# Kernel tuning notes

Measured on AMD Instinct MI355X. Metric: run time of the kernel, lower is better.

Reference implementation:

```python
import jax, jax.numpy as jnp
import numpy as np

N, E, D_IN, D_OUT = 100000, 1250000, 64, 100


def setup_inputs() -> dict:
    key = jax.random.key(0)
    ks = jax.random.split(key, 12)
    inp = {
        "x": jax.random.normal(ks[0], (N, D_IN), dtype=jnp.float32),
        "edge_index": jax.random.randint(ks[1], (2, E), 0, N, dtype=jnp.int64),
        "edge_weight": jax.random.uniform(ks[2], (E,), dtype=jnp.float32),
        # ChebConv(64,100,K=1): one weight + bias
        "W10": jax.random.normal(ks[3], (D_IN, D_OUT), dtype=jnp.float32) * 0.1,
        "b1": jnp.zeros((D_OUT,), dtype=jnp.float32),
        # ChebConv(64,100,K=2)
        "W20": jax.random.normal(ks[4], (D_IN, D_OUT), dtype=jnp.float32) * 0.1,
        "W21": jax.random.normal(ks[5], (D_IN, D_OUT), dtype=jnp.float32) * 0.1,
        "b2": jnp.zeros((D_OUT,), dtype=jnp.float32),
        # ChebConv(64,100,K=3)
        "W30": jax.random.normal(ks[6], (D_IN, D_OUT), dtype=jnp.float32) * 0.1,
        "W31": jax.random.normal(ks[7], (D_IN, D_OUT), dtype=jnp.float32) * 0.1,
        "W32": jax.random.normal(ks[8], (D_IN, D_OUT), dtype=jnp.float32) * 0.1,
        "b3": jnp.zeros((D_OUT,), dtype=jnp.float32),
    }
    return inp


def _cheb_norm(edge_index, edge_weight, n):
    # PyG ChebConv.__norm__ with normalization='sym', lambda_max=2.0:
    # L_hat = (2/lambda_max) * (I - D^-1/2 A D^-1/2) - I = -D^-1/2 A D^-1/2
    # (the +1 diagonal of L and the -1 self-loop cancel), diag entries are 0.
    row, col = edge_index[0], edge_index[1]
    deg = jax.ops.segment_sum(edge_weight, row, num_segments=n)
    dis = jnp.where(deg > 0, jax.lax.rsqrt(jnp.where(deg > 0, deg, 1.0)), 0.0)
    return -dis[row] * edge_weight * dis[col]


def _cheb_conv(x, edge_index, w_hat, weights, bias):
    # out = sum_k T_k(L_hat) x @ W_k + b, with T0=x, T1=Lx, T_k=2L T_{k-1}-T_{k-2}
    n = x.shape[0]
    row, col = edge_index[0], edge_index[1]

    def prop(t):  # L_hat @ t via edge gather/scatter
        return jax.ops.segment_sum(t[row] * w_hat[:, None], col, num_segments=n)

    tx0 = x
    out = tx0 @ weights[0]
    if len(weights) > 1:
        tx1 = prop(tx0)
        out = out + tx1 @ weights[1]
        for k in range(2, len(weights)):
            tx2 = 2.0 * prop(tx1) - tx0
            out = out + tx2 @ weights[k]
            tx0, tx1 = tx1, tx2
    return out + bias


def reference(x, edge_index, edge_weight, W10, b1, W20, W21, b2, W30, W31, W32, b3):
    w_hat = _cheb_norm(edge_index, edge_weight, x.shape[0])
    s1 = _cheb_conv(x, edge_index, w_hat, [W10], b1)
    s2 = _cheb_conv(x, edge_index, w_hat, [W20, W21], b2)
    s3 = _cheb_conv(x, edge_index, w_hat, [W30, W31, W32], b3)
    return jnp.concatenate([s1, s2, s3], axis=1)  # [N, 300]
```

## Files before the change

kernel.cpp:

```cpp
#include <hip/hip_runtime.h>


typedef __attribute__((ext_vector_type(8))) short short8;
typedef __attribute__((ext_vector_type(8))) unsigned short ushort8;
typedef __attribute__((ext_vector_type(4))) float f32x4;

#define NSBMAX 64
#define NSPLIT 16
#define NSPLIT_ROW 8

__device__ inline float bf2f(unsigned short u) {
    return __uint_as_float(((unsigned int)u) << 16);
}
__device__ inline unsigned short f2bf(float f) {
    unsigned int u = __float_as_uint(f);
    u = (u + 0x7FFF + ((u >> 16) & 1)) >> 16;
    return (unsigned short)u;
}

__global__ __launch_bounds__(512) void partA_kernel(
        const int* __restrict__ row, const int* __restrict__ col,
        const float* __restrict__ ew, int* __restrict__ colAcur,
        int* __restrict__ rowAcur, uint2* __restrict__ colA,
        uint2* __restrict__ rowA, int E, int nsb, int chunk, int capA) {
    __shared__ int hc[NSBMAX];
    __shared__ int hr[NSBMAX];
    const int t = threadIdx.x;
    const int s = blockIdx.x * chunk;
    const int e = min(E, s + chunk);
    if (s >= E) return;
    if (t < NSBMAX) { hc[t] = 0; hr[t] = 0; }
    __syncthreads();
    for (int i = s + t; i < e; i += 512) {
        atomicAdd(&hc[col[i] >> 11], 1);
        atomicAdd(&hr[row[i] >> 11], 1);
    }
    __syncthreads();
    if (t < nsb) {
        int n = hc[t];
        hc[t] = n ? atomicAdd(&colAcur[t], n) : 0;
        n = hr[t];
        hr[t] = n ? atomicAdd(&rowAcur[t], n) : 0;
    }
    __syncthreads();
    for (int i = s + t; i < e; i += 512) {
        int r = row[i], c = col[i];
        float w = ew[i];
        int pc = atomicAdd(&hc[c >> 11], 1);
        if (pc < capA)
            colA[(size_t)(c >> 11) * capA + pc] =
                make_uint2(((unsigned)(c & 2047) << 17) | (unsigned)r, __float_as_uint(w));
        int pr = atomicAdd(&hr[r >> 11], 1);
        if (pr < capA)
            rowA[(size_t)(r >> 11) * capA + pr] = make_uint2((unsigned)r, __float_as_uint(w));
    }
}

__global__ __launch_bounds__(512) void partB_kernel(
        const int* __restrict__ colAcur, const uint2* __restrict__ colA,
        int* __restrict__ colBcur, uint2* __restrict__ colB,
        int capA, int capB) {
    __shared__ int h[8];
    const int sb = blockIdx.x / NSPLIT;
    const int j = blockIdx.x % NSPLIT;
    const int t = threadIdx.x;
    const int cnt = min(colAcur[sb], capA);
    const int chunk = (cnt + NSPLIT - 1) / NSPLIT;
    const int s = j * chunk;
    const int e = min(cnt, s + chunk);
    if (t < 8) h[t] = 0;
    __syncthreads();
    const uint2* part = colA + (size_t)sb * capA;
    for (int i = s + t; i < e; i += 512) atomicAdd(&h[part[i].x >> 25], 1);
    __syncthreads();
    if (t < 8) {
        int n = h[t];
        h[t] = n ? atomicAdd(&colBcur[sb * 8 + t], n) : 0;
    }
    __syncthreads();
    for (int i = s + t; i < e; i += 512) {
        uint2 rec = part[i];
        int f = rec.x >> 25;
        int p = atomicAdd(&h[f], 1);
        if (p < capB) {
            unsigned coff = (rec.x >> 17) & 255u;
            unsigned r = rec.x & 0x1FFFFu;
            colB[(size_t)(sb * 8 + f) * capB + p] = make_uint2((coff << 24) | r, rec.y);
        }
    }
}

__global__ __launch_bounds__(512) void fine_rowp_kernel(
        const int* __restrict__ rowAcur, const uint2* __restrict__ rowA,
        float* __restrict__ partial, int capA) {
    __shared__ float sdeg[2048];
    const int sb = blockIdx.x / NSPLIT_ROW;
    const int j = blockIdx.x % NSPLIT_ROW;
    const int t = threadIdx.x;
    const int cnt = min(rowAcur[sb], capA);
    const int chunk = (cnt + NSPLIT_ROW - 1) / NSPLIT_ROW;
    const int s = j * chunk;
    const int e = min(cnt, s + chunk);
    for (int k = t; k < 2048; k += 512) sdeg[k] = 0.f;
    __syncthreads();
    const uint2* part = rowA + (size_t)sb * capA;
    for (int i = s + t; i < e; i += 512) {
        uint2 rec = part[i];
        atomicAdd(&sdeg[rec.x & 2047u], __uint_as_float(rec.y));
    }
    __syncthreads();
    float* dstp = partial + (size_t)blockIdx.x * 2048;
    for (int k = t; k < 2048; k += 512) dstp[k] = sdeg[k];
}

__global__ void colbase_scan_kernel(const int* __restrict__ colBcur,
                                    int* __restrict__ colbase,
                                    int* __restrict__ rowptr, int N, int nfb, int capB) {
    __shared__ int s[512];
    int t = threadIdx.x;
    int v = (t < nfb) ? min(colBcur[t], capB) : 0;
    s[t] = v;
    __syncthreads();
    for (int o = 1; o < 512; o <<= 1) {
        int u = (t >= o) ? s[t - o] : 0;
        __syncthreads();
        s[t] += u;
        __syncthreads();
    }
    if (t < nfb) colbase[t] = s[t] - v;
    if (t == 511) rowptr[N] = s[511];
}

__global__ __launch_bounds__(256) void fine_col_kernel(
        const int* __restrict__ colBcur, const int* __restrict__ colbase,
        const uint2* __restrict__ colB, const float* __restrict__ dis,
        uint2* __restrict__ erec, int* __restrict__ rowptr, int N, int capB) {
    __shared__ int h[256];
    __shared__ int sc[256];
    __shared__ int cur[256];
    const int b = blockIdx.x, t = threadIdx.x;
    const int sz = min(colBcur[b], capB);
    const uint2* part = colB + (size_t)b * capB;
    h[t] = 0;
    __syncthreads();
    for (int i = t; i < sz; i += 256) atomicAdd(&h[part[i].x >> 24], 1);
    __syncthreads();
    int v = h[t];
    sc[t] = v;
    __syncthreads();
    for (int o = 1; o < 256; o <<= 1) {
        int u = (t >= o) ? sc[t - o] : 0;
        __syncthreads();
        sc[t] += u;
        __syncthreads();
    }
    int excl = sc[t] - v;
    const int base = colbase[b];
    int c = (b << 8) + t;
    if (c < N) rowptr[c] = base + excl;
    cur[t] = excl;
    __syncthreads();
    for (int i = t; i < sz; i += 256) {
        uint2 rec = part[i];
        int coff = rec.x >> 24;
        int r = rec.x & 0xFFFFFFu;
        int pos = atomicAdd(&cur[coff], 1);
        float wd = __uint_as_float(rec.y) * dis[r];
        erec[(size_t)base + pos] = make_uint2((unsigned)r, __float_as_uint(wd));
    }
}

__global__ void deg_count_kernel(const int* __restrict__ row, const int* __restrict__ col,
                                 const float* __restrict__ ew,
                                 float* __restrict__ deg, int* __restrict__ cnt, int E) {
    int e = blockIdx.x * 256 + threadIdx.x;
    if (e < E) {
        atomicAdd(&deg[row[e]], ew[e]);
        atomicAdd(&cnt[col[e]], 1);
    }
}

__global__ void scan1_kernel(const int* __restrict__ cnt, int* __restrict__ pre,
                             int* __restrict__ bsum, int N) {
    __shared__ int s[256];
    int t = threadIdx.x;
    int i = blockIdx.x * 256 + t;
    int v = (i < N) ? cnt[i] : 0;
    s[t] = v;
    __syncthreads();
    for (int o = 1; o < 256; o <<= 1) {
        int u = (t >= o) ? s[t - o] : 0;
        __syncthreads();
        s[t] += u;
        __syncthreads();
    }
    if (i < N) pre[i] = s[t] - v;
    if (t == 255) bsum[blockIdx.x] = s[255];
}

__global__ void scan2_kernel(const int* __restrict__ bsum, int* __restrict__ bpre, int nb) {
    __shared__ int s[512];
    int t = threadIdx.x;
    int v = (t < nb) ? bsum[t] : 0;
    s[t] = v;
    __syncthreads();
    for (int o = 1; o < 512; o <<= 1) {
        int u = (t >= o) ? s[t - o] : 0;
        __syncthreads();
        s[t] += u;
        __syncthreads();
    }
    if (t < nb) bpre[t] = s[t] - v;
}

__global__ void scan3_kernel(int* __restrict__ rowptr, int* __restrict__ cursor,
                             const int* __restrict__ bpre, int N, int E) {
    int i = blockIdx.x * 256 + threadIdx.x;
    if (i < N) {
        int v = rowptr[i] + bpre[i >> 8];
        rowptr[i] = v;
        cursor[i] = v;
    }
    if (i == 0) rowptr[N] = E;
}

__global__ void scatter_compact_kernel(const int* __restrict__ row, const int* __restrict__ col,
                                       const float* __restrict__ ew, int* __restrict__ cursor,
                                       uint2* __restrict__ erec, int E) {
    int e = blockIdx.x * 256 + threadIdx.x;
    if (e < E) {
        int p = atomicAdd(&cursor[col[e]], 1);
        erec[p] = make_uint2((unsigned)row[e], __float_as_uint(ew[e]));
    }
}

__global__ void cvt_dis_kernel(const float* __restrict__ x, unsigned short* __restrict__ xb,
                               const float* __restrict__ degp, float* __restrict__ dis,
                               int N, int total4, int mode) {
    int i = blockIdx.x * 256 + threadIdx.x;
    if (i < total4) {
        float4 v = reinterpret_cast<const float4*>(x)[i];
        ushort4 o;
        o.x = f2bf(v.x); o.y = f2bf(v.y); o.z = f2bf(v.z); o.w = f2bf(v.w);
        reinterpret_cast<ushort4*>(xb)[i] = o;
    }
    if (mode && i < N) {
        float d;
        if (mode == 2) {
            const float* p = degp + ((size_t)(i >> 11) * NSPLIT_ROW) * 2048 + (i & 2047);
            d = 0.f;
#pragma unroll
            for (int j = 0; j < NSPLIT_ROW; ++j) d += p[(size_t)j * 2048];
        } else {
            d = degp[i];
        }
        dis[i] = (d > 0.f) ? rsqrtf(d) : 0.f;
    }
}

__global__ void gather_kernel(const int* __restrict__ ptr, const uint2* __restrict__ erec,
                              const float* __restrict__ dis,
                              const unsigned short* __restrict__ src,
                              unsigned short* __restrict__ dst, int N, int premul) {
    int node = blockIdx.x * 4 + (threadIdx.x >> 6);
    int lane = threadIdx.x & 63;
    if (node >= N) return;
    int s = ptr[node];
    int d = ptr[node + 1] - s;
    const int h = lane >> 5;
    const int c2 = (lane & 31) * 2;
    float acc0 = 0.f, acc1 = 0.f;
    for (int base = 0; base < d; base += 64) {
        int n = min(64, d - base);
        int ex = 0;
        float w = 0.f;
        if (lane < n) {
            uint2 e = erec[s + base + lane];
            ex = (int)e.x;
            w = __uint_as_float(e.y);
            if (!premul) w *= dis[ex];
        }
        int n8 = (n + 7) & ~7;
        for (int j = 0; j < n8; j += 8) {
            int r0 = __shfl(ex, j + 0, 64), r1 = __shfl(ex, j + 1, 64);
            int r2 = __shfl(ex, j + 2, 64), r3 = __shfl(ex, j + 3, 64);
            int r4 = __shfl(ex, j + 4, 64), r5 = __shfl(ex, j + 5, 64);
            int r6 = __shfl(ex, j + 6, 64), r7 = __shfl(ex, j + 7, 64);
            float w0 = __shfl(w, j + 0, 64), w1 = __shfl(w, j + 1, 64);
            float w2 = __shfl(w, j + 2, 64), w3 = __shfl(w, j + 3, 64);
            float w4 = __shfl(w, j + 4, 64), w5 = __shfl(w, j + 5, 64);
            float w6 = __shfl(w, j + 6, 64), w7 = __shfl(w, j + 7, 64);
            int ra = h ? r1 : r0;  float wa = h ? w1 : w0;
            int rb = h ? r3 : r2;  float wb = h ? w3 : w2;
            int rc = h ? r5 : r4;  float wc = h ? w5 : w4;
            int rd = h ? r7 : r6;  float wd = h ? w7 : w6;
            unsigned va = *reinterpret_cast<const unsigned*>(src + (size_t)ra * 64 + c2);
            unsigned vb = *reinterpret_cast<const unsigned*>(src + (size_t)rb * 64 + c2);
            unsigned vc = *reinterpret_cast<const unsigned*>(src + (size_t)rc * 64 + c2);
            unsigned vd = *reinterpret_cast<const unsigned*>(src + (size_t)rd * 64 + c2);
            acc0 = fmaf(wa, bf2f((unsigned short)(va & 0xFFFFu)), acc0);
            acc1 = fmaf(wa, bf2f((unsigned short)(va >> 16)), acc1);
            acc0 = fmaf(wb, bf2f((unsigned short)(vb & 0xFFFFu)), acc0);
            acc1 = fmaf(wb, bf2f((unsigned short)(vb >> 16)), acc1);
            acc0 = fmaf(wc, bf2f((unsigned short)(vc & 0xFFFFu)), acc0);
            acc1 = fmaf(wc, bf2f((unsigned short)(vc >> 16)), acc1);
            acc0 = fmaf(wd, bf2f((unsigned short)(vd & 0xFFFFu)), acc0);
            acc1 = fmaf(wd, bf2f((unsigned short)(vd >> 16)), acc1);
        }
    }
    acc0 += __shfl_xor(acc0, 32, 64);
    acc1 += __shfl_xor(acc1, 32, 64);
    if (lane < 32) {
        float sc = -dis[node];
        unsigned o = (unsigned)f2bf(sc * acc0) | ((unsigned)f2bf(sc * acc1) << 16);
        *reinterpret_cast<unsigned*>(dst + (size_t)node * 64 + c2) = o;
    }
}

__global__ void prep_w_kernel(const float* __restrict__ W10, const float* __restrict__ W20,
                              const float* __restrict__ W21, const float* __restrict__ W30,
                              const float* __restrict__ W31, const float* __restrict__ W32,
                              unsigned short* __restrict__ imgW) {
    int i = blockIdx.x * 256 + threadIdx.x;
    if (i >= 6 * 7168) return;
    int img = i / 7168;
    int rem = i - img * 7168;
    int j = rem & 7;
    int l = (rem >> 3) & 63;
    int ks = (rem >> 9) & 1;
    int t = rem >> 10;
    const float* W;
    switch (img) {
        case 0: W = W10; break;
        case 1: W = W20; break;
        case 2: W = W21; break;
        case 3: W = W30; break;
        case 4: W = W31; break;
        default: W = W32; break;
    }
    int n = t * 16 + (l & 15);
    int k = ks * 32 + (l >> 4) * 8 + j;
    float v = (n < 100) ? W[k * 100 + n] : 0.f;
    imgW[i] = f2bf(v);
}

#define PRODUCT(AF, IMGOFF, SEGBASE)                                                   \
    do {                                                                               \
        _Pragma("unroll") for (int ks = 0; ks < 2; ++ks) {                             \
            _Pragma("unroll") for (int t = 0; t < 7; ++t) {                            \
                short8 bfr = *reinterpret_cast<const short8*>(                         \
                    imgW + (IMGOFF) + ((t * 2 + ks) << 9) + (l << 3));                 \
                acc[(SEGBASE) + t] = __builtin_amdgcn_mfma_f32_16x16x32_bf16(          \
                    bfr, AF[ks], acc[(SEGBASE) + t], 0, 0, 0);                         \
            }                                                                          \
        }                                                                              \
    } while (0)

__global__ __launch_bounds__(256) void gemm_fused_kernel(
        const unsigned short* __restrict__ xb, const unsigned short* __restrict__ tx1b,
        const unsigned short* __restrict__ p2b, const unsigned short* __restrict__ imgW,
        const float* __restrict__ b1, const float* __restrict__ b2,
        const float* __restrict__ b3, float* __restrict__ out, int N) {
    __shared__ unsigned short Ftx[64 * 64];
    __shared__ unsigned short Ft1[64 * 64];
    __shared__ unsigned short Ft2[64 * 64];
    const int row0 = blockIdx.x * 64;
    const int tid = threadIdx.x;
    const int wv = tid >> 6;
    const int l = tid & 63;
    const int m = l & 15;
    const int q = l >> 4;

    f32x4 acc[21];
#pragma unroll
    for (int t = 0; t < 21; ++t) acc[t] = (f32x4){0.f, 0.f, 0.f, 0.f};

#pragma unroll
    for (int it = 0; it < 2; ++it) {
        int i = tid + it * 256;
        int r = i >> 3, g = i & 7;
        int grow = row0 + r;
        ushort8 vx = {0, 0, 0, 0, 0, 0, 0, 0};
        ushort8 v1 = vx, v2 = vx;
        if (grow < N) {
            vx = *reinterpret_cast<const ushort8*>(xb + (size_t)grow * 64 + g * 8);
            v1 = *reinterpret_cast<const ushort8*>(tx1b + (size_t)grow * 64 + g * 8);
            ushort8 vp = *reinterpret_cast<const ushort8*>(p2b + (size_t)grow * 64 + g * 8);
#pragma unroll
            for (int jj = 0; jj < 8; ++jj)
                v2[jj] = f2bf(2.f * bf2f(vp[jj]) - bf2f(vx[jj]));
        }
        int off = r * 64 + ((g ^ (r & 7)) << 3);
        *reinterpret_cast<ushort8*>(&Ftx[off]) = vx;
        *reinterpret_cast<ushort8*>(&Ft1[off]) = v1;
        *reinterpret_cast<ushort8*>(&Ft2[off]) = v2;
    }
    __syncthreads();

    const int arow = wv * 16 + m;
    short8 ax[2], a1[2], a2[2];
#pragma unroll
    for (int ks = 0; ks < 2; ++ks) {
        int o = arow * 64 + (((ks * 4 + q) ^ (arow & 7)) << 3);
        ax[ks] = *reinterpret_cast<const short8*>(&Ftx[o]);
        a1[ks] = *reinterpret_cast<const short8*>(&Ft1[o]);
        a2[ks] = *reinterpret_cast<const short8*>(&Ft2[o]);
    }

    PRODUCT(ax, 0, 0);
    PRODUCT(ax, 7168, 7);
    PRODUCT(a1, 14336, 7);
    PRODUCT(ax, 21504, 14);
    PRODUCT(a1, 28672, 14);
    PRODUCT(a2, 35840, 14);

    const int grow = row0 + wv * 16 + m;
    if (grow < N) {
        float* orow = out + (size_t)grow * 300;
#pragma unroll
        for (int seg = 0; seg < 3; ++seg) {
            const float* bs = (seg == 0) ? b1 : (seg == 1) ? b2 : b3;
#pragma unroll
            for (int t = 0; t < 7; ++t) {
                int c0 = t * 16 + q * 4;
                if (c0 + 3 >= 100) continue;
                float4 bv = *reinterpret_cast<const float4*>(bs + c0);
                f32x4 a = acc[seg * 7 + t];
                float4 o = make_float4(a[0] + bv.x, a[1] + bv.y, a[2] + bv.z, a[3] + bv.w);
                *reinterpret_cast<float4*>(orow + seg * 100 + c0) = o;
            }
        }
    }
}

extern "C" void kernel_launch(void* const* d_in, const int* in_sizes, int n_in,
                              void* d_out, int out_size, void* d_ws, size_t ws_size,
                              hipStream_t stream) {
    const float* x   = (const float*)d_in[0];
    const int*   ei  = (const int*)d_in[1];
    const float* ew  = (const float*)d_in[2];
    const float* W10 = (const float*)d_in[3];
    const float* b1  = (const float*)d_in[4];
    const float* W20 = (const float*)d_in[5];
    const float* W21 = (const float*)d_in[6];
    const float* b2  = (const float*)d_in[7];
    const float* W30 = (const float*)d_in[8];
    const float* W31 = (const float*)d_in[9];
    const float* W32 = (const float*)d_in[10];
    const float* b3  = (const float*)d_in[11];
    float* out = (float*)d_out;

    const int N = in_sizes[0] / 64;
    const int E = in_sizes[2];
    const int* row = ei;
    const int* col = ei + E;
    const int nb = (N + 255) / 256;
    const int eb = (E + 255) / 256;

    const int NSB = (N + 2047) >> 11;
    const int nfb = NSB * 8;

    int total4 = N * 16;
    int pg = (N + 3) / 4;
    int ntile = (N + 63) / 64;

    long meanA = ((long)E * 2048 + N - 1) / N;
    int capA = (int)(meanA + meanA / 4 + 1024);
    long meanB = ((long)E * 256 + N - 1) / N;
    int capB = (int)(meanB + meanB / 4 + 512);

    char* base = (char*)d_ws;
    size_t off = 0;
    auto alloc = [&](size_t bytes) { size_t o = off; off = (off + bytes + 15) & ~(size_t)15; return o; };

    float* dis           = (float*)(base + alloc((size_t)4 * N));
    int*   rowptr        = (int*)(base + alloc((size_t)4 * (N + 1)));
    int*   colAcur       = (int*)(base + alloc((size_t)4 * 640));
    int*   rowAcur       = colAcur + 64;
    int*   colBcur       = colAcur + 128;
    int*   colbase       = (int*)(base + alloc((size_t)4 * 512));
    unsigned short* xb   = (unsigned short*)(base + alloc((size_t)128 * N));
    unsigned short* tx1b = (unsigned short*)(base + alloc((size_t)128 * N));
    unsigned short* p2b  = (unsigned short*)(base + alloc((size_t)128 * N));
    unsigned short* imgW = (unsigned short*)(base + alloc((size_t)2 * 6 * 7168));
    uint2* erec          = (uint2*)(base + alloc((size_t)8 * E));
    size_t mainfix = off;
    uint2* colA          = (uint2*)(base + alloc((size_t)8 * NSB * capA));
    uint2* rowA          = (uint2*)(base + alloc((size_t)8 * NSB * capA));
    uint2* colB          = (uint2*)(base + alloc((size_t)8 * nfb * capB));
    float* partial       = (float*)(base + alloc((size_t)4 * NSB * NSPLIT_ROW * 2048));
    size_t mainneed = off;

    bool mainok = (N <= 131072) && (NSB <= NSBMAX) && (nfb <= 512) && (mainneed <= ws_size);

    if (mainok) {
        const int PBLK = 1024;
        int chunkA = (E + PBLK - 1) / PBLK;

        hipMemsetAsync(colAcur, 0, (size_t)4 * 640, stream);
        partA_kernel<<<PBLK, 512, 0, stream>>>(row, col, ew, colAcur, rowAcur,
                                               colA, rowA, E, NSB, chunkA, capA);
        partB_kernel<<<NSB * NSPLIT, 512, 0, stream>>>(colAcur, colA, colBcur, colB,
                                                       capA, capB);
        fine_rowp_kernel<<<NSB * NSPLIT_ROW, 512, 0, stream>>>(rowAcur, rowA, partial, capA);
        cvt_dis_kernel<<<(total4 + 255) / 256, 256, 0, stream>>>(x, xb, partial, dis,
                                                                 N, total4, 2);
        colbase_scan_kernel<<<1, 512, 0, stream>>>(colBcur, colbase, rowptr, N, nfb, capB);
        fine_col_kernel<<<nfb, 256, 0, stream>>>(colBcur, colbase, colB, dis,
                                                 erec, rowptr, N, capB);
        prep_w_kernel<<<(6 * 7168 + 255) / 256, 256, 0, stream>>>(W10, W20, W21, W30, W31, W32, imgW);

        gather_kernel<<<pg, 256, 0, stream>>>(rowptr, erec, dis, xb, tx1b, N, 1);
        gather_kernel<<<pg, 256, 0, stream>>>(rowptr, erec, dis, tx1b, p2b, N, 1);
        gemm_fused_kernel<<<ntile, 256, 0, stream>>>(xb, tx1b, p2b, imgW, b1, b2, b3, out, N);
    } else {
        off = mainfix;
        float* deg    = (float*)(base + alloc((size_t)4 * N));
        int*   cursor = (int*)(base + alloc((size_t)4 * N));
        int*   bsum   = (int*)(base + alloc((size_t)4 * nb));
        int*   bpre   = (int*)(base + alloc((size_t)4 * nb));

        hipMemsetAsync(deg, 0, (size_t)4 * N, stream);
        hipMemsetAsync(cursor, 0, (size_t)4 * N, stream);
        deg_count_kernel<<<eb, 256, 0, stream>>>(row, col, ew, deg, cursor, E);
        scan1_kernel<<<nb, 256, 0, stream>>>(cursor, rowptr, bsum, N);
        scan2_kernel<<<1, 512, 0, stream>>>(bsum, bpre, nb);
        scan3_kernel<<<nb, 256, 0, stream>>>(rowptr, cursor, bpre, N, E);
        scatter_compact_kernel<<<eb, 256, 0, stream>>>(row, col, ew, cursor, erec, E);
        cvt_dis_kernel<<<(total4 + 255) / 256, 256, 0, stream>>>(x, xb, deg, dis, N, total4, 1);
        prep_w_kernel<<<(6 * 7168 + 255) / 256, 256, 0, stream>>>(W10, W20, W21, W30, W31, W32, imgW);

        gather_kernel<<<pg, 256, 0, stream>>>(rowptr, erec, dis, xb, tx1b, N, 0);
        gather_kernel<<<pg, 256, 0, stream>>>(rowptr, erec, dis, tx1b, p2b, N, 0);
        gemm_fused_kernel<<<ntile, 256, 0, stream>>>(xb, tx1b, p2b, imgW, b1, b2, b3, out, N);
    }
}
```

Baseline: 388.5 us.

## Merge preprocessing kernels into three launches and move dis scaling into gather

Independent preprocessing kernels are packed into three launches by dispatching on block index. Weight prep rides with the edge partitioning pass, the column split rides with the row-degree partials, and the bf16 convert plus dis computation ride with the fine column bucketing. Each fine block now recomputes the column-base scan itself, so the separate scan kernel goes away. Because dis is no longer ready when edge records are written, the multiply by dis[row] moves into both gather passes, which adds a dependent load per edge in the hot loop in exchange for fewer launches and dependency bubbles.

```diff
diff --git a/kernel.cpp b/kernel.cpp
--- a/kernel.cpp
+++ b/kernel.cpp
@@ -18,14 +18,42 @@
     return (unsigned short)u;
 }
 
-__global__ __launch_bounds__(512) void partA_kernel(
+__global__ __launch_bounds__(512) void mergeA_kernel(
         const int* __restrict__ row, const int* __restrict__ col,
         const float* __restrict__ ew, int* __restrict__ colAcur,
         int* __restrict__ rowAcur, uint2* __restrict__ colA,
-        uint2* __restrict__ rowA, int E, int nsb, int chunk, int capA) {
+        uint2* __restrict__ rowA, int E, int nsb, int chunk, int capA, int pblk,
+        const float* __restrict__ W10, const float* __restrict__ W20,
+        const float* __restrict__ W21, const float* __restrict__ W30,
+        const float* __restrict__ W31, const float* __restrict__ W32,
+        unsigned short* __restrict__ imgW) {
     __shared__ int hc[NSBMAX];
     __shared__ int hr[NSBMAX];
     const int t = threadIdx.x;
+    if ((int)blockIdx.x >= pblk) {
+        int i = (blockIdx.x - pblk) * 512 + t;
+        if (i >= 6 * 7168) return;
+        int img = i / 7168;
+        int rem = i - img * 7168;
+        int j = rem & 7;
+        int l = (rem >> 3) & 63;
+        int ks = (rem >> 9) & 1;
+        int tt = rem >> 10;
+        const float* W;
+        switch (img) {
+            case 0: W = W10; break;
+            case 1: W = W20; break;
+            case 2: W = W21; break;
+            case 3: W = W30; break;
+            case 4: W = W31; break;
+            default: W = W32; break;
+        }
+        int n = tt * 16 + (l & 15);
+        int k = ks * 32 + (l >> 4) * 8 + j;
+        float v = (n < 100) ? W[k * 100 + n] : 0.f;
+        imgW[i] = f2bf(v);
+        return;
+    }
     const int s = blockIdx.x * chunk;
     const int e = min(E, s + chunk);
     if (s >= E) return;
@@ -56,117 +84,130 @@
     }
 }
 
-__global__ __launch_bounds__(512) void partB_kernel(
+__global__ __launch_bounds__(512) void mergeB_kernel(
         const int* __restrict__ colAcur, const uint2* __restrict__ colA,
         int* __restrict__ colBcur, uint2* __restrict__ colB,
-        int capA, int capB) {
-    __shared__ int h[8];
-    const int sb = blockIdx.x / NSPLIT;
-    const int j = blockIdx.x % NSPLIT;
+        int capA, int capB, int npartb,
+        const int* __restrict__ rowAcur, const uint2* __restrict__ rowA,
+        float* __restrict__ partial) {
+    __shared__ float smem[2048];
     const int t = threadIdx.x;
-    const int cnt = min(colAcur[sb], capA);
-    const int chunk = (cnt + NSPLIT - 1) / NSPLIT;
-    const int s = j * chunk;
-    const int e = min(cnt, s + chunk);
-    if (t < 8) h[t] = 0;
-    __syncthreads();
-    const uint2* part = colA + (size_t)sb * capA;
-    for (int i = s + t; i < e; i += 512) atomicAdd(&h[part[i].x >> 25], 1);
-    __syncthreads();
-    if (t < 8) {
-        int n = h[t];
-        h[t] = n ? atomicAdd(&colBcur[sb * 8 + t], n) : 0;
-    }
-    __syncthreads();
-    for (int i = s + t; i < e; i += 512) {
-        uint2 rec = part[i];
-        int f = rec.x >> 25;
-        int p = atomicAdd(&h[f], 1);
-        if (p < capB) {
-            unsigned coff = (rec.x >> 17) & 255u;
-            unsigned r = rec.x & 0x1FFFFu;
-            colB[(size_t)(sb * 8 + f) * capB + p] = make_uint2((coff << 24) | r, rec.y);
-        }
-    }
-}
-
-__global__ __launch_bounds__(512) void fine_rowp_kernel(
-        const int* __restrict__ rowAcur, const uint2* __restrict__ rowA,
-        float* __restrict__ partial, int capA) {
-    __shared__ float sdeg[2048];
-    const int sb = blockIdx.x / NSPLIT_ROW;
-    const int j = blockIdx.x % NSPLIT_ROW;
+    if ((int)blockIdx.x < npartb) {
+        int* h = (int*)smem;
+        const int sb = blockIdx.x / NSPLIT;
+        const int j = blockIdx.x % NSPLIT;
+        const int cnt = min(colAcur[sb], capA);
+        const int chunk = (cnt + NSPLIT - 1) / NSPLIT;
+        const int s = j * chunk;
+        const int e = min(cnt, s + chunk);
+        if (t < 8) h[t] = 0;
+        __syncthreads();
+        const uint2* part = colA + (size_t)sb * capA;
+        for (int i = s + t; i < e; i += 512) atomicAdd(&h[part[i].x >> 25], 1);
+        __syncthreads();
+        if (t < 8) {
+            int n = h[t];
+            h[t] = n ? atomicAdd(&colBcur[sb * 8 + t], n) : 0;
+        }
+        __syncthreads();
+        for (int i = s + t; i < e; i += 512) {
+            uint2 rec = part[i];
+            int f = rec.x >> 25;
+            int p = atomicAdd(&h[f], 1);
+            if (p < capB) {
+                unsigned coff = (rec.x >> 17) & 255u;
+                unsigned r = rec.x & 0x1FFFFu;
+                colB[(size_t)(sb * 8 + f) * capB + p] = make_uint2((coff << 24) | r, rec.y);
+            }
+        }
+    } else {
+        const int bid = blockIdx.x - npartb;
+        const int sb = bid / NSPLIT_ROW;
+        const int j = bid % NSPLIT_ROW;
+        const int cnt = min(rowAcur[sb], capA);
+        const int chunk = (cnt + NSPLIT_ROW - 1) / NSPLIT_ROW;
+        const int s = j * chunk;
+        const int e = min(cnt, s + chunk);
+        for (int k = t; k < 2048; k += 512) smem[k] = 0.f;
+        __syncthreads();
+        const uint2* part = rowA + (size_t)sb * capA;
+        for (int i = s + t; i < e; i += 512) {
+            uint2 rec = part[i];
+            atomicAdd(&smem[rec.x & 2047u], __uint_as_float(rec.y));
+        }
+        __syncthreads();
+        float* dstp = partial + (size_t)bid * 2048;
+        for (int k = t; k < 2048; k += 512) dstp[k] = smem[k];
+    }
+}
+
+__global__ __launch_bounds__(512) void mergeC_kernel(
+        const float* __restrict__ x, unsigned short* __restrict__ xb,
+        const float* __restrict__ degp, float* __restrict__ dis,
+        int N, int total4, int cvtb,
+        const int* __restrict__ colBcur, const uint2* __restrict__ colB,
+        uint2* __restrict__ erec, int* __restrict__ rowptr, int capB, int nfb) {
     const int t = threadIdx.x;
-    const int cnt = min(rowAcur[sb], capA);
-    const int chunk = (cnt + NSPLIT_ROW - 1) / NSPLIT_ROW;
-    const int s = j * chunk;
-    const int e = min(cnt, s + chunk);
-    for (int k = t; k < 2048; k += 512) sdeg[k] = 0.f;
-    __syncthreads();
-    const uint2* part = rowA + (size_t)sb * capA;
-    for (int i = s + t; i < e; i += 512) {
-        uint2 rec = part[i];
-        atomicAdd(&sdeg[rec.x & 2047u], __uint_as_float(rec.y));
-    }
-    __syncthreads();
-    float* dstp = partial + (size_t)blockIdx.x * 2048;
-    for (int k = t; k < 2048; k += 512) dstp[k] = sdeg[k];
-}
-
-__global__ void colbase_scan_kernel(const int* __restrict__ colBcur,
-                                    int* __restrict__ colbase,
-                                    int* __restrict__ rowptr, int N, int nfb, int capB) {
-    __shared__ int s[512];
-    int t = threadIdx.x;
-    int v = (t < nfb) ? min(colBcur[t], capB) : 0;
-    s[t] = v;
-    __syncthreads();
-    for (int o = 1; o < 512; o <<= 1) {
-        int u = (t >= o) ? s[t - o] : 0;
-        __syncthreads();
-        s[t] += u;
-        __syncthreads();
-    }
-    if (t < nfb) colbase[t] = s[t] - v;
-    if (t == 511) rowptr[N] = s[511];
-}
-
-__global__ __launch_bounds__(256) void fine_col_kernel(
-        const int* __restrict__ colBcur, const int* __restrict__ colbase,
-        const uint2* __restrict__ colB, const float* __restrict__ dis,
-        uint2* __restrict__ erec, int* __restrict__ rowptr, int N, int capB) {
+    if ((int)blockIdx.x < cvtb) {
+        int i = blockIdx.x * 512 + t;
+        if (i < total4) {
+            float4 v = reinterpret_cast<const float4*>(x)[i];
+            ushort4 o;
+            o.x = f2bf(v.x); o.y = f2bf(v.y); o.z = f2bf(v.z); o.w = f2bf(v.w);
+            reinterpret_cast<ushort4*>(xb)[i] = o;
+        }
+        if (i < N) {
+            const float* p = degp + ((size_t)(i >> 11) * NSPLIT_ROW) * 2048 + (i & 2047);
+            float d = 0.f;
+#pragma unroll
+            for (int j = 0; j < NSPLIT_ROW; ++j) d += p[(size_t)j * 2048];
+            dis[i] = (d > 0.f) ? rsqrtf(d) : 0.f;
+        }
+        return;
+    }
+    __shared__ int s512[512];
     __shared__ int h[256];
     __shared__ int sc[256];
     __shared__ int cur[256];
-    const int b = blockIdx.x, t = threadIdx.x;
+    const int b = blockIdx.x - cvtb;
+    int v0 = (t < nfb) ? min(colBcur[t], capB) : 0;
+    s512[t] = v0;
+    __syncthreads();
+    for (int o = 1; o < 512; o <<= 1) {
+        int u = (t >= o) ? s512[t - o] : 0;
+        __syncthreads();
+        s512[t] += u;
+        __syncthreads();
+    }
+    const int base = (b > 0) ? s512[b - 1] : 0;
+    if (b == 0 && t == 0) rowptr[N] = s512[511];
     const int sz = min(colBcur[b], capB);
     const uint2* part = colB + (size_t)b * capB;
-    h[t] = 0;
-    __syncthreads();
-    for (int i = t; i < sz; i += 256) atomicAdd(&h[part[i].x >> 24], 1);
-    __syncthreads();
-    int v = h[t];
-    sc[t] = v;
+    if (t < 256) h[t] = 0;
+    __syncthreads();
+    for (int i = t; i < sz; i += 512) atomicAdd(&h[part[i].x >> 24], 1);
+    __syncthreads();
+    if (t < 256) sc[t] = h[t];
     __syncthreads();
     for (int o = 1; o < 256; o <<= 1) {
-        int u = (t >= o) ? sc[t - o] : 0;
-        __syncthreads();
-        sc[t] += u;
-        __syncthreads();
-    }
-    int excl = sc[t] - v;
-    const int base = colbase[b];
-    int c = (b << 8) + t;
-    if (c < N) rowptr[c] = base + excl;
-    cur[t] = excl;
-    __syncthreads();
-    for (int i = t; i < sz; i += 256) {
+        int u = (t < 256 && t >= o) ? sc[t - o] : 0;
+        __syncthreads();
+        if (t < 256) sc[t] += u;
+        __syncthreads();
+    }
+    if (t < 256) {
+        int excl = sc[t] - h[t];
+        int c = (b << 8) + t;
+        if (c < N) rowptr[c] = base + excl;
+        cur[t] = excl;
+    }
+    __syncthreads();
+    for (int i = t; i < sz; i += 512) {
         uint2 rec = part[i];
         int coff = rec.x >> 24;
         int r = rec.x & 0xFFFFFFu;
         int pos = atomicAdd(&cur[coff], 1);
-        float wd = __uint_as_float(rec.y) * dis[r];
-        erec[(size_t)base + pos] = make_uint2((unsigned)r, __float_as_uint(wd));
+        erec[(size_t)base + pos] = make_uint2((unsigned)r, rec.y);
     }
 }
 
@@ -235,8 +276,8 @@
 }
 
 __global__ void cvt_dis_kernel(const float* __restrict__ x, unsigned short* __restrict__ xb,
-                               const float* __restrict__ degp, float* __restrict__ dis,
-                               int N, int total4, int mode) {
+                               const float* __restrict__ deg, float* __restrict__ dis,
+                               int N, int total4) {
     int i = blockIdx.x * 256 + threadIdx.x;
     if (i < total4) {
         float4 v = reinterpret_cast<const float4*>(x)[i];
@@ -244,24 +285,43 @@
         o.x = f2bf(v.x); o.y = f2bf(v.y); o.z = f2bf(v.z); o.w = f2bf(v.w);
         reinterpret_cast<ushort4*>(xb)[i] = o;
     }
-    if (mode && i < N) {
-        float d;
-        if (mode == 2) {
-            const float* p = degp + ((size_t)(i >> 11) * NSPLIT_ROW) * 2048 + (i & 2047);
-            d = 0.f;
-#pragma unroll
-            for (int j = 0; j < NSPLIT_ROW; ++j) d += p[(size_t)j * 2048];
-        } else {
-            d = degp[i];
-        }
+    if (i < N) {
+        float d = deg[i];
         dis[i] = (d > 0.f) ? rsqrtf(d) : 0.f;
     }
+}
+
+__global__ void prep_w_kernel(const float* __restrict__ W10, const float* __restrict__ W20,
+                              const float* __restrict__ W21, const float* __restrict__ W30,
+                              const float* __restrict__ W31, const float* __restrict__ W32,
+                              unsigned short* __restrict__ imgW) {
+    int i = blockIdx.x * 256 + threadIdx.x;
+    if (i >= 6 * 7168) return;
+    int img = i / 7168;
+    int rem = i - img * 7168;
+    int j = rem & 7;
+    int l = (rem >> 3) & 63;
+    int ks = (rem >> 9) & 1;
+    int t = rem >> 10;
+    const float* W;
+    switch (img) {
+        case 0: W = W10; break;
+        case 1: W = W20; break;
+        case 2: W = W21; break;
+        case 3: W = W30; break;
+        case 4: W = W31; break;
+        default: W = W32; break;
+    }
+    int n = t * 16 + (l & 15);
+    int k = ks * 32 + (l >> 4) * 8 + j;
+    float v = (n < 100) ? W[k * 100 + n] : 0.f;
+    imgW[i] = f2bf(v);
 }
 
 __global__ void gather_kernel(const int* __restrict__ ptr, const uint2* __restrict__ erec,
                               const float* __restrict__ dis,
                               const unsigned short* __restrict__ src,
-                              unsigned short* __restrict__ dst, int N, int premul) {
+                              unsigned short* __restrict__ dst, int N) {
     int node = blockIdx.x * 4 + (threadIdx.x >> 6);
     int lane = threadIdx.x & 63;
     if (node >= N) return;
@@ -277,8 +337,7 @@
         if (lane < n) {
             uint2 e = erec[s + base + lane];
             ex = (int)e.x;
-            w = __uint_as_float(e.y);
-            if (!premul) w *= dis[ex];
+            w = __uint_as_float(e.y) * dis[ex];
         }
         int n8 = (n + 7) & ~7;
         for (int j = 0; j < n8; j += 8) {
@@ -317,33 +376,6 @@
     }
 }
 
-__global__ void prep_w_kernel(const float* __restrict__ W10, const float* __restrict__ W20,
-                              const float* __restrict__ W21, const float* __restrict__ W30,
-                              const float* __restrict__ W31, const float* __restrict__ W32,
-                              unsigned short* __restrict__ imgW) {
-    int i = blockIdx.x * 256 + threadIdx.x;
-    if (i >= 6 * 7168) return;
-    int img = i / 7168;
-    int rem = i - img * 7168;
-    int j = rem & 7;
-    int l = (rem >> 3) & 63;
-    int ks = (rem >> 9) & 1;
-    int t = rem >> 10;
-    const float* W;
-    switch (img) {
-        case 0: W = W10; break;
-        case 1: W = W20; break;
-        case 2: W = W21; break;
-        case 3: W = W30; break;
-        case 4: W = W31; break;
-        default: W = W32; break;
-    }
-    int n = t * 16 + (l & 15);
-    int k = ks * 32 + (l >> 4) * 8 + j;
-    float v = (n < 100) ? W[k * 100 + n] : 0.f;
-    imgW[i] = f2bf(v);
-}
-
 #define PRODUCT(AF, IMGOFF, SEGBASE)                                                   \
     do {                                                                               \
         _Pragma("unroll") for (int ks = 0; ks < 2; ++ks) {                             \
@@ -478,7 +510,6 @@
     int*   colAcur       = (int*)(base + alloc((size_t)4 * 640));
     int*   rowAcur       = colAcur + 64;
     int*   colBcur       = colAcur + 128;
-    int*   colbase       = (int*)(base + alloc((size_t)4 * 512));
     unsigned short* xb   = (unsigned short*)(base + alloc((size_t)128 * N));
     unsigned short* tx1b = (unsigned short*)(base + alloc((size_t)128 * N));
     unsigned short* p2b  = (unsigned short*)(base + alloc((size_t)128 * N));
@@ -496,22 +527,21 @@
     if (mainok) {
         const int PBLK = 1024;
         int chunkA = (E + PBLK - 1) / PBLK;
+        int prepB = (6 * 7168 + 511) / 512;
+        int cvtB = (total4 + 511) / 512;
 
         hipMemsetAsync(colAcur, 0, (size_t)4 * 640, stream);
-        partA_kernel<<<PBLK, 512, 0, stream>>>(row, col, ew, colAcur, rowAcur,
-                                               colA, rowA, E, NSB, chunkA, capA);
-        partB_kernel<<<NSB * NSPLIT, 512, 0, stream>>>(colAcur, colA, colBcur, colB,
-                                                       capA, capB);
-        fine_rowp_kernel<<<NSB * NSPLIT_ROW, 512, 0, stream>>>(rowAcur, rowA, partial, capA);
-        cvt_dis_kernel<<<(total4 + 255) / 256, 256, 0, stream>>>(x, xb, partial, dis,
-                                                                 N, total4, 2);
-        colbase_scan_kernel<<<1, 512, 0, stream>>>(colBcur, colbase, rowptr, N, nfb, capB);
-        fine_col_kernel<<<nfb, 256, 0, stream>>>(colBcur, colbase, colB, dis,
-                                                 erec, rowptr, N, capB);
-        prep_w_kernel<<<(6 * 7168 + 255) / 256, 256, 0, stream>>>(W10, W20, W21, W30, W31, W32, imgW);
-
-        gather_kernel<<<pg, 256, 0, stream>>>(rowptr, erec, dis, xb, tx1b, N, 1);
-        gather_kernel<<<pg, 256, 0, stream>>>(rowptr, erec, dis, tx1b, p2b, N, 1);
+        mergeA_kernel<<<PBLK + prepB, 512, 0, stream>>>(
+            row, col, ew, colAcur, rowAcur, colA, rowA, E, NSB, chunkA, capA, PBLK,
+            W10, W20, W21, W30, W31, W32, imgW);
+        mergeB_kernel<<<NSB * NSPLIT + NSB * NSPLIT_ROW, 512, 0, stream>>>(
+            colAcur, colA, colBcur, colB, capA, capB, NSB * NSPLIT,
+            rowAcur, rowA, partial);
+        mergeC_kernel<<<cvtB + nfb, 512, 0, stream>>>(
+            x, xb, partial, dis, N, total4, cvtB,
+            colBcur, colB, erec, rowptr, capB, nfb);
+        gather_kernel<<<pg, 256, 0, stream>>>(rowptr, erec, dis, xb, tx1b, N);
+        gather_kernel<<<pg, 256, 0, stream>>>(rowptr, erec, dis, tx1b, p2b, N);
         gemm_fused_kernel<<<ntile, 256, 0, stream>>>(xb, tx1b, p2b, imgW, b1, b2, b3, out, N);
     } else {
         off = mainfix;
@@ -527,11 +557,11 @@
         scan2_kernel<<<1, 512, 0, stream>>>(bsum, bpre, nb);
         scan3_kernel<<<nb, 256, 0, stream>>>(rowptr, cursor, bpre, N, E);
         scatter_compact_kernel<<<eb, 256, 0, stream>>>(row, col, ew, cursor, erec, E);
-        cvt_dis_kernel<<<(total4 + 255) / 256, 256, 0, stream>>>(x, xb, deg, dis, N, total4, 1);
+        cvt_dis_kernel<<<(total4 + 255) / 256, 256, 0, stream>>>(x, xb, deg, dis, N, total4);
         prep_w_kernel<<<(6 * 7168 + 255) / 256, 256, 0, stream>>>(W10, W20, W21, W30, W31, W32, imgW);
 
-        gather_kernel<<<pg, 256, 0, stream>>>(rowptr, erec, dis, xb, tx1b, N, 0);
-        gather_kernel<<<pg, 256, 0, stream>>>(rowptr, erec, dis, tx1b, p2b, N, 0);
+        gather_kernel<<<pg, 256, 0, stream>>>(rowptr, erec, dis, xb, tx1b, N);
+        gather_kernel<<<pg, 256, 0, stream>>>(rowptr, erec, dis, tx1b, p2b, N);
         gemm_fused_kernel<<<ntile, 256, 0, stream>>>(xb, tx1b, p2b, imgW, b1, b2, b3, out, N);
     }
 }
```

After: 396.4 us. +2.0%, slower.
